# Kernel optimization log

Measured on AMD Instinct MI355X. Metric: run time of the kernel, lower is better.

Reference implementation:

```python
import jax, jax.numpy as jnp
import numpy as np

NUM_HEADS = 8
SIZE_Q = 512
SIZE_K = 512
SIZE_V = 512
B, S = 2, 2048


def setup_inputs() -> dict:
    key = jax.random.key(0)
    ks = jax.random.split(key, 16)
    Hk = SIZE_K  # num_heads * head_size_k
    Hv = SIZE_V  # num_heads * head_size_v
    inp = {
        "k": jax.random.normal(ks[0], (B, S, SIZE_K), jnp.float32),
        "v": jax.random.normal(ks[1], (B, S, SIZE_V), jnp.float32),
        "q": jax.random.normal(ks[2], (B, S, SIZE_Q), jnp.float32),
        "mask": jax.random.randint(ks[3], (S, S), 0, 2).astype(jnp.bool_),
        "spatial_bias": jax.random.normal(ks[4], (1, NUM_HEADS, S, S), jnp.float32),
        # Linear params stored as [in, out]; y = x @ W + b
        "Wq": jax.random.normal(ks[5], (SIZE_Q, Hk), jnp.float32) / np.sqrt(SIZE_Q),
        "bq": jnp.zeros((Hk,), jnp.float32),
        "Wk": jax.random.normal(ks[6], (SIZE_K, Hk), jnp.float32) / np.sqrt(SIZE_K),
        "bk": jnp.zeros((Hk,), jnp.float32),
        "Wv": jax.random.normal(ks[7], (SIZE_V, Hv), jnp.float32) / np.sqrt(SIZE_V),
        "bv": jnp.zeros((Hv,), jnp.float32),
        "Wo": jax.random.normal(ks[8], (Hv, SIZE_V), jnp.float32) / np.sqrt(Hv),
        "bo": jnp.zeros((SIZE_V,), jnp.float32),
    }
    return inp


def reference(k, v, q, mask, spatial_bias, Wq, bq, Wk, bk, Wv, bv, Wo, bo):
    batch, sk = k.shape[0], k.shape[1]
    sq = q.shape[1]
    hdk = Wk.shape[1] // NUM_HEADS
    hdv = Wv.shape[1] // NUM_HEADS
    # QKV projections -> [B, H, S, hd]
    kp = (k @ Wk + bk).reshape(batch, sk, NUM_HEADS, hdk).transpose(0, 2, 1, 3)
    vp = (v @ Wv + bv).reshape(batch, sk, NUM_HEADS, hdv).transpose(0, 2, 1, 3)
    qp = (q @ Wq + bq).reshape(batch, sq, NUM_HEADS, hdk).transpose(0, 2, 1, 3)
    qp = qp / jnp.sqrt(jnp.asarray(hdk, qp.dtype))
    # Scores with additive spatial bias and boolean mask (2D mask -> [1,1,S,S])
    scores = jnp.einsum("bhqd,bhkd->bhqk", qp, kp) + spatial_bias
    scores = jnp.where(mask[None, None, :, :], scores, -jnp.inf)
    attn = jax.nn.softmax(scores, axis=-1)  # dropout=0 (eval)
    ctx = jnp.einsum("bhqk,bhkd->bhqd", attn, vp)
    ctx = ctx.transpose(0, 2, 1, 3).reshape(batch, sq, NUM_HEADS * hdv)
    return ctx @ Wo + bo
```

## Files before the change

kernel.cpp:

```cpp
#include <hip/hip_runtime.h>
#include <hip/hip_bf16.h>

#define S_LEN 2048
#define NH 8
#define HD 64
#define CH 512
#define NEG_BIG (-3.0e38f)

typedef __bf16 bf16;
typedef bf16 bf16x8 __attribute__((ext_vector_type(8)));
typedef bf16 bf16x4 __attribute__((ext_vector_type(4)));
typedef float floatx4 __attribute__((ext_vector_type(4)));

__global__ void detect_mask_kernel(const unsigned char* __restrict__ mb,
                                   int* __restrict__ flag_out) {
    __shared__ int s1, s3;
    if (threadIdx.x == 0) { s1 = 0; s3 = 0; }
    __syncthreads();
    int any1 = 0, any3 = 0;
    int base = threadIdx.x * 16;
    for (int i = base; i < base + 16; ++i) {
        unsigned char bch = mb[i];
        int m = i & 3;
        if (bch != 0) {
            if (m == 1) any1 = 1;
            if (m == 2 || m == 3) any3 = 1;
        }
    }
    if (any1) atomicOr(&s1, 1);
    if (any3) atomicOr(&s3, 1);
    __syncthreads();
    if (threadIdx.x == 0) {
        int f = 0;
        if (s1) f = 1;
        else if (s3) f = 2;
        *flag_out = f;
    }
}

__global__ __launch_bounds__(256) void prep_weights_kernel(
    const float* __restrict__ Wq, const float* __restrict__ Wk,
    const float* __restrict__ Wv, const float* __restrict__ Wo,
    bf16* __restrict__ WThi, bf16* __restrict__ WTlo)
{
    __shared__ float tile[64][65];
    const int t = threadIdx.x;
    const int n0 = blockIdx.x * 64;
    const int k0 = blockIdx.y * 64;
    const int mat = blockIdx.z;
    const float* W = (mat == 0) ? Wq : (mat == 1) ? Wk : (mat == 2) ? Wv : Wo;
    bf16* hi = WThi + (size_t)mat * (CH * CH);
    bf16* lo = WTlo + (size_t)mat * (CH * CH);
#pragma unroll
    for (int i = 0; i < 4; ++i) {
        int row = (t >> 4) + 16 * i;
        int c4 = (t & 15) << 2;
        float4 f = *(const float4*)(W + (size_t)(k0 + row) * CH + n0 + c4);
        tile[row][c4 + 0] = f.x; tile[row][c4 + 1] = f.y;
        tile[row][c4 + 2] = f.z; tile[row][c4 + 3] = f.w;
    }
    __syncthreads();
#pragma unroll
    for (int i = 0; i < 4; ++i) {
        int nr = (t >> 4) + 16 * i;
        int k4 = (t & 15) << 2;
        bf16x4 h, l;
#pragma unroll
        for (int j = 0; j < 4; ++j) {
            float x = tile[k4 + j][nr];
            bf16 hv = (bf16)x;
            h[j] = hv;
            l[j] = (bf16)(x - (float)hv);
        }
        *(bf16x4*)(hi + (size_t)(n0 + nr) * CH + k0 + k4) = h;
        *(bf16x4*)(lo + (size_t)(n0 + nr) * CH + k0 + k4) = l;
    }
}

__device__ __forceinline__ void gemm_bf16_tile(
    bf16* __restrict__ As_hi, bf16* __restrict__ As_lo,
    bf16* __restrict__ Bs_hi, bf16* __restrict__ Bs_lo,
    const float* __restrict__ IN, const bf16* __restrict__ WThi,
    const bf16* __restrict__ WTlo, const float* __restrict__ BI,
    float* __restrict__ OUT, float scale, int mode)
{
    const int t = threadIdx.x;
    const int w = t >> 6;
    const int lane = t & 63;
    const int m16 = lane & 15;
    const int quad = lane >> 4;
    const int m0 = blockIdx.y * 128;
    const int n0 = blockIdx.x * 128;

    const int arow = t >> 1;
    const int akc  = (t & 1) << 4;

    floatx4 acc[2][8];
#pragma unroll
    for (int mi = 0; mi < 2; ++mi)
#pragma unroll
        for (int ni = 0; ni < 8; ++ni) {
            acc[mi][ni][0] = 0.f; acc[mi][ni][1] = 0.f;
            acc[mi][ni][2] = 0.f; acc[mi][ni][3] = 0.f;
        }

    float4 af[4];
    bf16x8 pbh[2], pbl[2];

    auto loadA = [&](int k0) {
        const float* p = IN + (size_t)(m0 + arow) * CH + k0 + akc;
        af[0] = ((const float4*)p)[0];
        af[1] = ((const float4*)p)[1];
        af[2] = ((const float4*)p)[2];
        af[3] = ((const float4*)p)[3];
    };
    auto loadB = [&](int k0) {
        const bf16* ph = WThi + (size_t)(n0 + arow) * CH + k0 + akc;
        const bf16* pl = WTlo + (size_t)(n0 + arow) * CH + k0 + akc;
        pbh[0] = ((const bf16x8*)ph)[0]; pbh[1] = ((const bf16x8*)ph)[1];
        pbl[0] = ((const bf16x8*)pl)[0]; pbl[1] = ((const bf16x8*)pl)[1];
    };
    auto stage = [&]() {
#pragma unroll
        for (int hh = 0; hh < 2; ++hh) {
            bf16x8 h, l;
#pragma unroll
            for (int j = 0; j < 8; ++j) {
                float x = ((const float*)&af[2 * hh])[j];
                bf16 hv = (bf16)x;
                h[j] = hv;
                l[j] = (bf16)(x - (float)hv);
            }
            *(bf16x8*)&As_hi[arow * 40 + akc + 8 * hh] = h;
            *(bf16x8*)&As_lo[arow * 40 + akc + 8 * hh] = l;
        }
        *(bf16x8*)&Bs_hi[arow * 40 + akc + 0] = pbh[0];
        *(bf16x8*)&Bs_hi[arow * 40 + akc + 8] = pbh[1];
        *(bf16x8*)&Bs_lo[arow * 40 + akc + 0] = pbl[0];
        *(bf16x8*)&Bs_lo[arow * 40 + akc + 8] = pbl[1];
    };

    loadA(0); loadB(0);
    for (int ks = 0; ks < CH / 32; ++ks) {
        __syncthreads();
        stage();
        __syncthreads();
        if (ks + 1 < CH / 32) { loadA(32 * (ks + 1)); loadB(32 * (ks + 1)); }

        bf16x8 bh[8], bl[8];
#pragma unroll
        for (int ni = 0; ni < 8; ++ni) {
            bh[ni] = *(const bf16x8*)&Bs_hi[(16 * ni + m16) * 40 + 8 * quad];
            bl[ni] = *(const bf16x8*)&Bs_lo[(16 * ni + m16) * 40 + 8 * quad];
        }
#pragma unroll
        for (int mi = 0; mi < 2; ++mi) {
            bf16x8 ah = *(const bf16x8*)&As_hi[(32 * w + 16 * mi + m16) * 40 + 8 * quad];
            bf16x8 al = *(const bf16x8*)&As_lo[(32 * w + 16 * mi + m16) * 40 + 8 * quad];
#pragma unroll
            for (int ni = 0; ni < 8; ++ni) {
                acc[mi][ni] = __builtin_amdgcn_mfma_f32_16x16x32_bf16(ah, bh[ni], acc[mi][ni], 0, 0, 0);
                acc[mi][ni] = __builtin_amdgcn_mfma_f32_16x16x32_bf16(ah, bl[ni], acc[mi][ni], 0, 0, 0);
                acc[mi][ni] = __builtin_amdgcn_mfma_f32_16x16x32_bf16(al, bh[ni], acc[mi][ni], 0, 0, 0);
            }
        }
    }

#pragma unroll
    for (int mi = 0; mi < 2; ++mi) {
#pragma unroll
        for (int r = 0; r < 4; ++r) {
            int row = m0 + 32 * w + 16 * mi + 4 * quad + r;
            int bb = row >> 11;
            int ss = row & (S_LEN - 1);
#pragma unroll
            for (int ni = 0; ni < 8; ++ni) {
                int col = n0 + 16 * ni + m16;
                float v = (acc[mi][ni][r] + BI[col]) * scale;
                if (mode == 0) {
                    int hh = col >> 6, dd = col & 63;
                    OUT[(((size_t)bb * NH + hh) * S_LEN + ss) * HD + dd] = v;
                } else if (mode == 1) {
                    int hh = col >> 6, dd = col & 63;
                    OUT[(((size_t)bb * NH + hh) * HD + dd) * S_LEN + ss] = v;
                } else {
                    OUT[(size_t)row * CH + col] = v;
                }
            }
        }
    }
}

__global__ __launch_bounds__(256, 2) void qkv_gemm_kernel(
    const float* __restrict__ q_in, const float* __restrict__ k_in,
    const float* __restrict__ v_in,
    const bf16* __restrict__ WThi, const bf16* __restrict__ WTlo,
    const float* __restrict__ bq, const float* __restrict__ bk,
    const float* __restrict__ bv,
    float* __restrict__ qp, float* __restrict__ kp, float* __restrict__ vpT)
{
    __shared__ __attribute__((aligned(16))) bf16 As_hi[128 * 40];
    __shared__ __attribute__((aligned(16))) bf16 As_lo[128 * 40];
    __shared__ __attribute__((aligned(16))) bf16 Bs_hi[128 * 40];
    __shared__ __attribute__((aligned(16))) bf16 Bs_lo[128 * 40];
    int z = blockIdx.z;
    if (z == 0)
        gemm_bf16_tile(As_hi, As_lo, Bs_hi, Bs_lo, q_in,
                       WThi, WTlo, bq, qp, 0.125f, 0);
    else if (z == 1)
        gemm_bf16_tile(As_hi, As_lo, Bs_hi, Bs_lo, k_in,
                       WThi + (size_t)CH * CH, WTlo + (size_t)CH * CH, bk, kp, 1.0f, 0);
    else
        gemm_bf16_tile(As_hi, As_lo, Bs_hi, Bs_lo, v_in,
                       WThi + (size_t)2 * CH * CH, WTlo + (size_t)2 * CH * CH, bv, vpT, 1.0f, 1);
}

__global__ __launch_bounds__(256, 2) void out_gemm_kernel(
    const float* __restrict__ ctx,
    const bf16* __restrict__ WThi, const bf16* __restrict__ WTlo,
    const float* __restrict__ bo, float* __restrict__ out)
{
    __shared__ __attribute__((aligned(16))) bf16 As_hi[128 * 40];
    __shared__ __attribute__((aligned(16))) bf16 As_lo[128 * 40];
    __shared__ __attribute__((aligned(16))) bf16 Bs_hi[128 * 40];
    __shared__ __attribute__((aligned(16))) bf16 Bs_lo[128 * 40];
    gemm_bf16_tile(As_hi, As_lo, Bs_hi, Bs_lo, ctx,
                   WThi + (size_t)3 * CH * CH, WTlo + (size_t)3 * CH * CH, bo, out, 1.0f, 2);
}

__global__ __launch_bounds__(256, 2) void attn_kernel(
    const float* __restrict__ qp, const float* __restrict__ kp,
    const float* __restrict__ vpT, const float* __restrict__ bias,
    const void* __restrict__ mask, const int* __restrict__ flagp,
    float* __restrict__ ctxb)
{
    __shared__ __attribute__((aligned(16))) bf16 Kbf[64 * 72];
    __shared__ __attribute__((aligned(16))) bf16 VsT[64 * 72];
    __shared__ __attribute__((aligned(16))) bf16 Pbf[64 * 72];
    __shared__ __attribute__((aligned(16))) float sbias[64 * 68];

    const int t    = threadIdx.x;
    const int w    = t >> 6;
    const int lane = t & 63;
    const int m    = lane & 15;
    const int quad = lane >> 4;
    const int q0   = blockIdx.x * 64;
    const int h    = blockIdx.y;
    const int b    = blockIdx.z;
    const int bh   = b * NH + h;
    const int flag = *flagp;

    bf16x8 qf[2];
    {
        const float* qrow =
            qp + ((size_t)bh * S_LEN + q0 + 16 * w + m) * HD + 8 * quad;
#pragma unroll
        for (int c = 0; c < 2; ++c) {
            float4 f0 = *(const float4*)(qrow + 32 * c);
            float4 f1 = *(const float4*)(qrow + 32 * c + 4);
            bf16x8 v;
            v[0] = (bf16)f0.x; v[1] = (bf16)f0.y; v[2] = (bf16)f0.z; v[3] = (bf16)f0.w;
            v[4] = (bf16)f1.x; v[5] = (bf16)f1.y; v[6] = (bf16)f1.z; v[7] = (bf16)f1.w;
            qf[c] = v;
        }
    }

    floatx4 ctx[4];
    float mrow[4], lrow[4];
#pragma unroll
    for (int tt = 0; tt < 4; ++tt) { ctx[tt][0]=0.f; ctx[tt][1]=0.f; ctx[tt][2]=0.f; ctx[tt][3]=0.f; }
#pragma unroll
    for (int r = 0; r < 4; ++r) { mrow[r] = NEG_BIG; lrow[r] = 0.f; }

    float4 kreg[4], vreg[4], breg[4];
    uint4  mreg[4];

    auto prefetch = [&](int k0) {
#pragma unroll
        for (int i = 0; i < 4; ++i) {
            int fl  = t + 256 * i;
            int row = fl >> 4;
            int c4  = (fl & 15) << 2;
            kreg[i] = *(const float4*)(kp  + ((size_t)bh * S_LEN + k0 + row) * HD + c4);
            vreg[i] = *(const float4*)(vpT + ((size_t)bh * HD + row) * S_LEN + k0 + c4);
            int grow = q0 + row;
            breg[i] = *(const float4*)(bias + ((size_t)h * S_LEN + grow) * S_LEN + k0 + c4);
            size_t mi0 = (size_t)grow * S_LEN + k0 + c4;
            if (flag == 1)
                mreg[i].x = *(const unsigned int*)((const unsigned char*)mask + mi0);
            else
                mreg[i] = *(const uint4*)((const unsigned int*)mask + mi0);
        }
    };
    auto stage = [&]() {
#pragma unroll
        for (int i = 0; i < 4; ++i) {
            int fl  = t + 256 * i;
            int row = fl >> 4;
            int c4  = (fl & 15) << 2;
            float4 kf = kreg[i], vf = vreg[i], bf = breg[i];
            bf16x4 kv, vv;
            kv[0] = (bf16)kf.x; kv[1] = (bf16)kf.y; kv[2] = (bf16)kf.z; kv[3] = (bf16)kf.w;
            vv[0] = (bf16)vf.x; vv[1] = (bf16)vf.y; vv[2] = (bf16)vf.z; vv[3] = (bf16)vf.w;
            *(bf16x4*)&Kbf[row * 72 + c4] = kv;
            *(bf16x4*)&VsT[row * 72 + c4] = vv;
            unsigned mj0, mj1, mj2, mj3;
            if (flag == 1) {
                unsigned mx = mreg[i].x;
                mj0 = mx & 255u; mj1 = (mx >> 8) & 255u;
                mj2 = (mx >> 16) & 255u; mj3 = mx >> 24;
            } else {
                mj0 = mreg[i].x; mj1 = mreg[i].y; mj2 = mreg[i].z; mj3 = mreg[i].w;
            }
            float4 sb;
            sb.x = mj0 ? bf.x : NEG_BIG;
            sb.y = mj1 ? bf.y : NEG_BIG;
            sb.z = mj2 ? bf.z : NEG_BIG;
            sb.w = mj3 ? bf.w : NEG_BIG;
            *(float4*)&sbias[row * 68 + c4] = sb;
        }
    };

    prefetch(0);
    for (int k0 = 0; k0 < S_LEN; k0 += 64) {
        __syncthreads();
        stage();
        __syncthreads();
        if (k0 + 64 < S_LEN) prefetch(k0 + 64);

        floatx4 sc[4];
#pragma unroll
        for (int tt = 0; tt < 4; ++tt) { sc[tt][0]=0.f; sc[tt][1]=0.f; sc[tt][2]=0.f; sc[tt][3]=0.f; }
#pragma unroll
        for (int st = 0; st < 2; ++st)
#pragma unroll
            for (int tt = 0; tt < 4; ++tt) {
                bf16x8 kf = *(const bf16x8*)&Kbf[(16 * tt + m) * 72 + 8 * quad + 32 * st];
                sc[tt] = __builtin_amdgcn_mfma_f32_16x16x32_bf16(qf[st], kf, sc[tt], 0, 0, 0);
            }

        float alpha[4];
#pragma unroll
        for (int r = 0; r < 4; ++r) {
            int lrowq = 16 * w + 4 * quad + r;
            float s[4];
#pragma unroll
            for (int tt = 0; tt < 4; ++tt)
                s[tt] = sc[tt][r] + sbias[lrowq * 68 + 16 * tt + m];
            float mx = fmaxf(fmaxf(s[0], s[1]), fmaxf(s[2], s[3]));
            mx = fmaxf(mx, __shfl_xor(mx, 1));
            mx = fmaxf(mx, __shfl_xor(mx, 2));
            mx = fmaxf(mx, __shfl_xor(mx, 4));
            mx = fmaxf(mx, __shfl_xor(mx, 8));
            float mnew = fmaxf(mrow[r], mx);
            float al = __expf(mrow[r] - mnew);
            float ls = 0.f;
#pragma unroll
            for (int tt = 0; tt < 4; ++tt) {
                float p = (s[tt] <= -1e37f) ? 0.f : __expf(s[tt] - mnew);
                ls += p;
                Pbf[lrowq * 72 + 16 * tt + m] = (bf16)p;
            }
            ls += __shfl_xor(ls, 1);
            ls += __shfl_xor(ls, 2);
            ls += __shfl_xor(ls, 4);
            ls += __shfl_xor(ls, 8);
            lrow[r] = lrow[r] * al + ls;
            mrow[r] = mnew;
            alpha[r] = al;
        }
#pragma unroll
        for (int tt = 0; tt < 4; ++tt)
#pragma unroll
            for (int r = 0; r < 4; ++r) ctx[tt][r] *= alpha[r];

#pragma unroll
        for (int st = 0; st < 2; ++st) {
            bf16x8 pf = *(const bf16x8*)&Pbf[(16 * w + m) * 72 + 8 * quad + 32 * st];
#pragma unroll
            for (int tt = 0; tt < 4; ++tt) {
                bf16x8 vf = *(const bf16x8*)&VsT[(16 * tt + m) * 72 + 8 * quad + 32 * st];
                ctx[tt] = __builtin_amdgcn_mfma_f32_16x16x32_bf16(pf, vf, ctx[tt], 0, 0, 0);
            }
        }
    }

#pragma unroll
    for (int r = 0; r < 4; ++r) {
        float inv = lrow[r] > 0.f ? 1.f / lrow[r] : 0.f;
        int grow = q0 + 16 * w + 4 * quad + r;
#pragma unroll
        for (int tt = 0; tt < 4; ++tt) {
            ctxb[((size_t)b * S_LEN + grow) * CH + h * HD + 16 * tt + m] =
                ctx[tt][r] * inv;
        }
    }
}

extern "C" void kernel_launch(void* const* d_in, const int* in_sizes, int n_in,
                              void* d_out, int out_size, void* d_ws, size_t ws_size,
                              hipStream_t stream) {
    const float* k_in = (const float*)d_in[0];
    const float* v_in = (const float*)d_in[1];
    const float* q_in = (const float*)d_in[2];
    const void*  mask = d_in[3];
    const float* bias = (const float*)d_in[4];
    const float* Wq = (const float*)d_in[5];
    const float* bq = (const float*)d_in[6];
    const float* Wk = (const float*)d_in[7];
    const float* bk = (const float*)d_in[8];
    const float* Wv = (const float*)d_in[9];
    const float* bv = (const float*)d_in[10];
    const float* Wo = (const float*)d_in[11];
    const float* bo = (const float*)d_in[12];
    float* out = (float*)d_out;

    float* wsf = (float*)d_ws;
    float* qp  = wsf;
    float* kp  = wsf + 2097152;
    float* vpT = wsf + 4194304;
    float* ctx = wsf + 6291456;
    bf16* WThi = (bf16*)(wsf + 8388608);
    bf16* WTlo = WThi + (size_t)4 * CH * CH;
    int*  flag = (int*)(WTlo + (size_t)4 * CH * CH);

    detect_mask_kernel<<<1, 256, 0, stream>>>((const unsigned char*)mask, flag);
    prep_weights_kernel<<<dim3(8, 8, 4), 256, 0, stream>>>(
        Wq, Wk, Wv, Wo, WThi, WTlo);
    qkv_gemm_kernel<<<dim3(4, 32, 3), 256, 0, stream>>>(
        q_in, k_in, v_in, WThi, WTlo, bq, bk, bv, qp, kp, vpT);
    attn_kernel<<<dim3(32, 8, 2), 256, 0, stream>>>(
        qp, kp, vpT, bias, mask, flag, ctx);
    out_gemm_kernel<<<dim3(4, 32, 1), 256, 0, stream>>>(
        ctx, WThi, WTlo, bo, out);
}
```

Measured before the change: 385.7 us.

## Split attention over key halves, pre-swizzle bf16 K/V, load via LDS DMA

The QKV GEMM now writes K and V directly as bf16 in XOR-swizzled layouts. The attention kernel streams these tiles into LDS with global_load_lds, which removes the per-tile fp32-to-bf16 staging and the padded shared buffers. Bias and mask are read straight into registers instead of going through a shared sbias tile. The key dimension is split in two (flash-decoding style), doubling the grid and raising occupancy to 4. A new merge kernel combines the partial results using the saved m/l statistics, at the cost of extra partial-context traffic and one more launch.

```diff
diff --git a/kernel.cpp b/kernel.cpp
--- a/kernel.cpp
+++ b/kernel.cpp
@@ -6,11 +6,19 @@
 #define HD 64
 #define CH 512
 #define NEG_BIG (-3.0e38f)
+#define SKSPLIT 2
+#define KHALF (S_LEN / SKSPLIT)
 
 typedef __bf16 bf16;
 typedef bf16 bf16x8 __attribute__((ext_vector_type(8)));
 typedef bf16 bf16x4 __attribute__((ext_vector_type(4)));
 typedef float floatx4 __attribute__((ext_vector_type(4)));
+
+typedef const unsigned int __attribute__((address_space(1)))* gas1_t;
+typedef unsigned int __attribute__((address_space(3)))* las3_t;
+__device__ __forceinline__ void gll16(const void* g, void* l) {
+    __builtin_amdgcn_global_load_lds((gas1_t)g, (las3_t)l, 16, 0, 0);
+}
 
 __global__ void detect_mask_kernel(const unsigned char* __restrict__ mb,
                                    int* __restrict__ flag_out) {
@@ -82,7 +90,7 @@
     bf16* __restrict__ Bs_hi, bf16* __restrict__ Bs_lo,
     const float* __restrict__ IN, const bf16* __restrict__ WThi,
     const bf16* __restrict__ WTlo, const float* __restrict__ BI,
-    float* __restrict__ OUT, float scale, int mode)
+    float* __restrict__ OUT, bf16* __restrict__ OBF, float scale, int mode)
 {
     const int t = threadIdx.x;
     const int w = t >> 6;
@@ -180,9 +188,14 @@
                 if (mode == 0) {
                     int hh = col >> 6, dd = col & 63;
                     OUT[(((size_t)bb * NH + hh) * S_LEN + ss) * HD + dd] = v;
-                } else if (mode == 1) {
+                } else if (mode == 3) {
                     int hh = col >> 6, dd = col & 63;
-                    OUT[(((size_t)bb * NH + hh) * HD + dd) * S_LEN + ss] = v;
+                    OBF[((size_t)(bb * NH + hh) * S_LEN + ss) * HD
+                        + (((dd >> 3) ^ (ss & 7)) << 3) + (dd & 7)] = (bf16)v;
+                } else if (mode == 4) {
+                    int hh = col >> 6, dd = col & 63;
+                    OBF[((size_t)(bb * NH + hh) * HD + dd) * S_LEN
+                        + (ss & ~63) + ((((ss >> 3) & 7) ^ (dd & 7)) << 3) + (ss & 7)] = (bf16)v;
                 } else {
                     OUT[(size_t)row * CH + col] = v;
                 }
@@ -197,7 +210,7 @@
     const bf16* __restrict__ WThi, const bf16* __restrict__ WTlo,
     const float* __restrict__ bq, const float* __restrict__ bk,
     const float* __restrict__ bv,
-    float* __restrict__ qp, float* __restrict__ kp, float* __restrict__ vpT)
+    float* __restrict__ qp, bf16* __restrict__ kswz, bf16* __restrict__ vswz)
 {
     __shared__ __attribute__((aligned(16))) bf16 As_hi[128 * 40];
     __shared__ __attribute__((aligned(16))) bf16 As_lo[128 * 40];
@@ -206,13 +219,15 @@
     int z = blockIdx.z;
     if (z == 0)
         gemm_bf16_tile(As_hi, As_lo, Bs_hi, Bs_lo, q_in,
-                       WThi, WTlo, bq, qp, 0.125f, 0);
+                       WThi, WTlo, bq, qp, nullptr, 0.125f, 0);
     else if (z == 1)
         gemm_bf16_tile(As_hi, As_lo, Bs_hi, Bs_lo, k_in,
-                       WThi + (size_t)CH * CH, WTlo + (size_t)CH * CH, bk, kp, 1.0f, 0);
+                       WThi + (size_t)CH * CH, WTlo + (size_t)CH * CH, bk,
+                       nullptr, kswz, 1.0f, 3);
     else
         gemm_bf16_tile(As_hi, As_lo, Bs_hi, Bs_lo, v_in,
-                       WThi + (size_t)2 * CH * CH, WTlo + (size_t)2 * CH * CH, bv, vpT, 1.0f, 1);
+                       WThi + (size_t)2 * CH * CH, WTlo + (size_t)2 * CH * CH, bv,
+                       nullptr, vswz, 1.0f, 4);
 }
 
 __global__ __launch_bounds__(256, 2) void out_gemm_kernel(
@@ -225,35 +240,38 @@
     __shared__ __attribute__((aligned(16))) bf16 Bs_hi[128 * 40];
     __shared__ __attribute__((aligned(16))) bf16 Bs_lo[128 * 40];
     gemm_bf16_tile(As_hi, As_lo, Bs_hi, Bs_lo, ctx,
-                   WThi + (size_t)3 * CH * CH, WTlo + (size_t)3 * CH * CH, bo, out, 1.0f, 2);
-}
-
-__global__ __launch_bounds__(256, 2) void attn_kernel(
-    const float* __restrict__ qp, const float* __restrict__ kp,
-    const float* __restrict__ vpT, const float* __restrict__ bias,
+                   WThi + (size_t)3 * CH * CH, WTlo + (size_t)3 * CH * CH, bo,
+                   out, nullptr, 1.0f, 2);
+}
+
+__global__ __launch_bounds__(256, 4) void attn_kernel(
+    const float* __restrict__ qp, const bf16* __restrict__ kswz,
+    const bf16* __restrict__ vswz, const float* __restrict__ bias,
     const void* __restrict__ mask, const int* __restrict__ flagp,
-    float* __restrict__ ctxb)
-{
-    __shared__ __attribute__((aligned(16))) bf16 Kbf[64 * 72];
-    __shared__ __attribute__((aligned(16))) bf16 VsT[64 * 72];
+    float* __restrict__ ctxp, float* __restrict__ ml)
+{
+    __shared__ __attribute__((aligned(16))) bf16 Kt[64 * 64];
+    __shared__ __attribute__((aligned(16))) bf16 Vt[64 * 64];
     __shared__ __attribute__((aligned(16))) bf16 Pbf[64 * 72];
-    __shared__ __attribute__((aligned(16))) float sbias[64 * 68];
 
     const int t    = threadIdx.x;
     const int w    = t >> 6;
     const int lane = t & 63;
-    const int m    = lane & 15;
+    const int m16  = lane & 15;
     const int quad = lane >> 4;
+    const int mx7  = m16 & 7;
     const int q0   = blockIdx.x * 64;
     const int h    = blockIdx.y;
-    const int b    = blockIdx.z;
+    const int b    = blockIdx.z >> 1;
+    const int kz   = blockIdx.z & 1;
     const int bh   = b * NH + h;
     const int flag = *flagp;
+    const int kbeg = kz * KHALF;
 
     bf16x8 qf[2];
     {
         const float* qrow =
-            qp + ((size_t)bh * S_LEN + q0 + 16 * w + m) * HD + 8 * quad;
+            qp + ((size_t)bh * S_LEN + q0 + 16 * w + m16) * HD + 8 * quad;
 #pragma unroll
         for (int c = 0; c < 2; ++c) {
             float4 f0 = *(const float4*)(qrow + 32 * c);
@@ -265,68 +283,60 @@
         }
     }
 
-    floatx4 ctx[4];
+    floatx4 ctxa[4];
     float mrow[4], lrow[4];
 #pragma unroll
-    for (int tt = 0; tt < 4; ++tt) { ctx[tt][0]=0.f; ctx[tt][1]=0.f; ctx[tt][2]=0.f; ctx[tt][3]=0.f; }
+    for (int tt = 0; tt < 4; ++tt) { ctxa[tt][0]=0.f; ctxa[tt][1]=0.f; ctxa[tt][2]=0.f; ctxa[tt][3]=0.f; }
 #pragma unroll
     for (int r = 0; r < 4; ++r) { mrow[r] = NEG_BIG; lrow[r] = 0.f; }
 
-    float4 kreg[4], vreg[4], breg[4];
-    uint4  mreg[4];
-
-    auto prefetch = [&](int k0) {
-#pragma unroll
-        for (int i = 0; i < 4; ++i) {
-            int fl  = t + 256 * i;
-            int row = fl >> 4;
-            int c4  = (fl & 15) << 2;
-            kreg[i] = *(const float4*)(kp  + ((size_t)bh * S_LEN + k0 + row) * HD + c4);
-            vreg[i] = *(const float4*)(vpT + ((size_t)bh * HD + row) * S_LEN + k0 + c4);
-            int grow = q0 + row;
-            breg[i] = *(const float4*)(bias + ((size_t)h * S_LEN + grow) * S_LEN + k0 + c4);
-            size_t mi0 = (size_t)grow * S_LEN + k0 + c4;
-            if (flag == 1)
-                mreg[i].x = *(const unsigned int*)((const unsigned char*)mask + mi0);
-            else
-                mreg[i] = *(const uint4*)((const unsigned int*)mask + mi0);
-        }
+    const int qrow0 = q0 + 16 * w + 4 * quad;
+    const float* bbase = bias + ((size_t)h * S_LEN + qrow0) * S_LEN + m16;
+    const unsigned char* mb8  = (const unsigned char*)mask + (size_t)qrow0 * S_LEN + m16;
+    const unsigned int*  mb32 = (const unsigned int*)mask  + (size_t)qrow0 * S_LEN + m16;
+
+    float bnext[16]; unsigned mnext[16]; float mb[16];
+    auto prefetchBM = [&](int k0) {
+        if (flag == 1) {
+#pragma unroll
+            for (int r = 0; r < 4; ++r)
+#pragma unroll
+                for (int tt = 0; tt < 4; ++tt)
+                    mnext[4 * r + tt] = mb8[(size_t)r * S_LEN + k0 + 16 * tt];
+        } else {
+#pragma unroll
+            for (int r = 0; r < 4; ++r)
+#pragma unroll
+                for (int tt = 0; tt < 4; ++tt)
+                    mnext[4 * r + tt] = mb32[(size_t)r * S_LEN + k0 + 16 * tt];
+        }
+#pragma unroll
+        for (int r = 0; r < 4; ++r)
+#pragma unroll
+            for (int tt = 0; tt < 4; ++tt)
+                bnext[4 * r + tt] = bbase[(size_t)r * S_LEN + k0 + 16 * tt];
     };
-    auto stage = [&]() {
-#pragma unroll
-        for (int i = 0; i < 4; ++i) {
-            int fl  = t + 256 * i;
-            int row = fl >> 4;
-            int c4  = (fl & 15) << 2;
-            float4 kf = kreg[i], vf = vreg[i], bf = breg[i];
-            bf16x4 kv, vv;
-            kv[0] = (bf16)kf.x; kv[1] = (bf16)kf.y; kv[2] = (bf16)kf.z; kv[3] = (bf16)kf.w;
-            vv[0] = (bf16)vf.x; vv[1] = (bf16)vf.y; vv[2] = (bf16)vf.z; vv[3] = (bf16)vf.w;
-            *(bf16x4*)&Kbf[row * 72 + c4] = kv;
-            *(bf16x4*)&VsT[row * 72 + c4] = vv;
-            unsigned mj0, mj1, mj2, mj3;
-            if (flag == 1) {
-                unsigned mx = mreg[i].x;
-                mj0 = mx & 255u; mj1 = (mx >> 8) & 255u;
-                mj2 = (mx >> 16) & 255u; mj3 = mx >> 24;
-            } else {
-                mj0 = mreg[i].x; mj1 = mreg[i].y; mj2 = mreg[i].z; mj3 = mreg[i].w;
-            }
-            float4 sb;
-            sb.x = mj0 ? bf.x : NEG_BIG;
-            sb.y = mj1 ? bf.y : NEG_BIG;
-            sb.z = mj2 ? bf.z : NEG_BIG;
-            sb.w = mj3 ? bf.w : NEG_BIG;
-            *(float4*)&sbias[row * 68 + c4] = sb;
-        }
-    };
-
-    prefetch(0);
-    for (int k0 = 0; k0 < S_LEN; k0 += 64) {
+    prefetchBM(kbeg);
+
+    const bf16* kb = kswz + (size_t)bh * S_LEN * HD;
+    const bf16* vb = vswz + (size_t)bh * HD * S_LEN;
+    const int lrow8 = lane >> 3;
+    const int lcol8 = (lane & 7) * 8;
+
+    for (int k0 = kbeg; k0 < kbeg + KHALF; k0 += 64) {
         __syncthreads();
-        stage();
+#pragma unroll
+        for (int i = 0; i < 2; ++i) {
+            int c = 2 * w + i;
+            int row = 8 * c + lrow8;
+            gll16(kb + (size_t)(k0 + row) * HD + lcol8, &Kt[c * 512]);
+            gll16(vb + (size_t)row * S_LEN + k0 + lcol8, &Vt[c * 512]);
+        }
         __syncthreads();
-        if (k0 + 64 < S_LEN) prefetch(k0 + 64);
+
+#pragma unroll
+        for (int j = 0; j < 16; ++j) mb[j] = mnext[j] ? bnext[j] : NEG_BIG;
+        if (k0 + 64 < kbeg + KHALF) prefetchBM(k0 + 64);
 
         floatx4 sc[4];
 #pragma unroll
@@ -335,7 +345,8 @@
         for (int st = 0; st < 2; ++st)
 #pragma unroll
             for (int tt = 0; tt < 4; ++tt) {
-                bf16x8 kf = *(const bf16x8*)&Kbf[(16 * tt + m) * 72 + 8 * quad + 32 * st];
+                bf16x8 kf = *(const bf16x8*)&Kt[(16 * tt + m16) * 64
+                                                + (((quad + 4 * st) ^ mx7) << 3)];
                 sc[tt] = __builtin_amdgcn_mfma_f32_16x16x32_bf16(qf[st], kf, sc[tt], 0, 0, 0);
             }
 
@@ -346,7 +357,7 @@
             float s[4];
 #pragma unroll
             for (int tt = 0; tt < 4; ++tt)
-                s[tt] = sc[tt][r] + sbias[lrowq * 68 + 16 * tt + m];
+                s[tt] = sc[tt][r] + mb[4 * r + tt];
             float mx = fmaxf(fmaxf(s[0], s[1]), fmaxf(s[2], s[3]));
             mx = fmaxf(mx, __shfl_xor(mx, 1));
             mx = fmaxf(mx, __shfl_xor(mx, 2));
@@ -359,7 +370,7 @@
             for (int tt = 0; tt < 4; ++tt) {
                 float p = (s[tt] <= -1e37f) ? 0.f : __expf(s[tt] - mnew);
                 ls += p;
-                Pbf[lrowq * 72 + 16 * tt + m] = (bf16)p;
+                Pbf[lrowq * 72 + 16 * tt + m16] = (bf16)p;
             }
             ls += __shfl_xor(ls, 1);
             ls += __shfl_xor(ls, 2);
@@ -372,29 +383,61 @@
 #pragma unroll
         for (int tt = 0; tt < 4; ++tt)
 #pragma unroll
-            for (int r = 0; r < 4; ++r) ctx[tt][r] *= alpha[r];
+            for (int r = 0; r < 4; ++r) ctxa[tt][r] *= alpha[r];
 
 #pragma unroll
         for (int st = 0; st < 2; ++st) {
-            bf16x8 pf = *(const bf16x8*)&Pbf[(16 * w + m) * 72 + 8 * quad + 32 * st];
+            bf16x8 pf = *(const bf16x8*)&Pbf[(16 * w + m16) * 72 + 8 * quad + 32 * st];
 #pragma unroll
             for (int tt = 0; tt < 4; ++tt) {
-                bf16x8 vf = *(const bf16x8*)&VsT[(16 * tt + m) * 72 + 8 * quad + 32 * st];
-                ctx[tt] = __builtin_amdgcn_mfma_f32_16x16x32_bf16(pf, vf, ctx[tt], 0, 0, 0);
-            }
-        }
-    }
-
+                bf16x8 vf = *(const bf16x8*)&Vt[(16 * tt + m16) * 64
+                                                + (((quad + 4 * st) ^ mx7) << 3)];
+                ctxa[tt] = __builtin_amdgcn_mfma_f32_16x16x32_bf16(pf, vf, ctxa[tt], 0, 0, 0);
+            }
+        }
+    }
+
+    float* cp = ctxp + (size_t)kz * (2 * NH * S_LEN * HD);
 #pragma unroll
     for (int r = 0; r < 4; ++r) {
-        float inv = lrow[r] > 0.f ? 1.f / lrow[r] : 0.f;
         int grow = q0 + 16 * w + 4 * quad + r;
-#pragma unroll
-        for (int tt = 0; tt < 4; ++tt) {
-            ctxb[((size_t)b * S_LEN + grow) * CH + h * HD + 16 * tt + m] =
-                ctx[tt][r] * inv;
-        }
-    }
+        size_t prow = (size_t)bh * S_LEN + grow;
+#pragma unroll
+        for (int tt = 0; tt < 4; ++tt)
+            cp[prow * HD + 16 * tt + m16] = ctxa[tt][r];
+        if (m16 == 0) {
+            ml[((size_t)kz * (2 * NH * S_LEN) + prow) * 2 + 0] = mrow[r];
+            ml[((size_t)kz * (2 * NH * S_LEN) + prow) * 2 + 1] = lrow[r];
+        }
+    }
+}
+
+__global__ __launch_bounds__(256) void merge_kernel(
+    const float* __restrict__ ctxp, const float* __restrict__ ml,
+    float* __restrict__ ctxo)
+{
+    const int PHALF = 2 * NH * S_LEN * HD;
+    const int MLHALF = 2 * NH * S_LEN;
+    int idx = blockIdx.x * 256 + threadIdx.x;
+    int d = (idx & 15) << 2;
+    int h = (idx >> 4) & (NH - 1);
+    int s = (idx >> 7) & (S_LEN - 1);
+    int b = idx >> 18;
+    size_t prow = ((size_t)b * NH + h) * S_LEN + s;
+    float m0 = ml[prow * 2],            l0 = ml[prow * 2 + 1];
+    float m1 = ml[(MLHALF + prow) * 2], l1 = ml[(MLHALF + prow) * 2 + 1];
+    float mx = fmaxf(m0, m1);
+    float a0 = __expf(m0 - mx), a1 = __expf(m1 - mx);
+    float den = a0 * l0 + a1 * l1;
+    float inv = den > 0.f ? 1.f / den : 0.f;
+    float4 c0 = *(const float4*)(ctxp + prow * HD + d);
+    float4 c1 = *(const float4*)(ctxp + PHALF + prow * HD + d);
+    float4 o;
+    o.x = (a0 * c0.x + a1 * c1.x) * inv;
+    o.y = (a0 * c0.y + a1 * c1.y) * inv;
+    o.z = (a0 * c0.z + a1 * c1.z) * inv;
+    o.w = (a0 * c0.w + a1 * c1.w) * inv;
+    *(float4*)(ctxo + ((size_t)b * S_LEN + s) * CH + h * HD + d) = o;
 }
 
 extern "C" void kernel_launch(void* const* d_in, const int* in_sizes, int n_in,
@@ -415,22 +458,25 @@
     const float* bo = (const float*)d_in[12];
     float* out = (float*)d_out;
 
-    float* wsf = (float*)d_ws;
-    float* qp  = wsf;
-    float* kp  = wsf + 2097152;
-    float* vpT = wsf + 4194304;
-    float* ctx = wsf + 6291456;
-    bf16* WThi = (bf16*)(wsf + 8388608);
-    bf16* WTlo = WThi + (size_t)4 * CH * CH;
-    int*  flag = (int*)(WTlo + (size_t)4 * CH * CH);
+    char* base = (char*)d_ws;
+    float* qp   = (float*)(base);
+    float* ctx  = (float*)(base);
+    float* ctxp = (float*)(base + (8u  << 20));
+    float* mlb  = (float*)(base + (24u << 20));
+    bf16*  kswz = (bf16*)(base + (25u << 20));
+    bf16*  vswz = (bf16*)(base + (29u << 20));
+    bf16*  WThi = (bf16*)(base + (33u << 20));
+    bf16*  WTlo = (bf16*)(base + (35u << 20));
+    int*   flag = (int*) (base + (37u << 20));
 
     detect_mask_kernel<<<1, 256, 0, stream>>>((const unsigned char*)mask, flag);
     prep_weights_kernel<<<dim3(8, 8, 4), 256, 0, stream>>>(
         Wq, Wk, Wv, Wo, WThi, WTlo);
     qkv_gemm_kernel<<<dim3(4, 32, 3), 256, 0, stream>>>(
-        q_in, k_in, v_in, WThi, WTlo, bq, bk, bv, qp, kp, vpT);
-    attn_kernel<<<dim3(32, 8, 2), 256, 0, stream>>>(
-        qp, kp, vpT, bias, mask, flag, ctx);
+        q_in, k_in, v_in, WThi, WTlo, bq, bk, bv, qp, kswz, vswz);
+    attn_kernel<<<dim3(32, 8, 2 * SKSPLIT), 256, 0, stream>>>(
+        qp, kswz, vswz, bias, mask, flag, ctxp, mlb);
+    merge_kernel<<<2048, 256, 0, stream>>>(ctxp, mlb, ctx);
     out_gemm_kernel<<<dim3(4, 32, 1), 256, 0, stream>>>(
         ctx, WThi, WTlo, bo, out);
 }
```

Result: no change. 379.6 us (-1.6%).
